# Optimization experiments

Measured on AMD Instinct MI355X. Metric: run time of the kernel, lower is better.

## Reference

```python
import jax, jax.numpy as jnp
import numpy as np

OC, IC, K, STRIDE, PAD, DIL, GROUPS = 256, 256, 3, 1, 1, 1, 1


def _conv_one(x, w):
    # x: [C, H, W], w: [OC, IC//groups, K, K]
    out = jax.lax.conv_general_dilated(
        x[None], w,
        window_strides=(STRIDE, STRIDE),
        padding=[(PAD, PAD), (PAD, PAD)],
        rhs_dilation=(DIL, DIL),
        dimension_numbers=("NCHW", "OIHW", "NCHW"),
        feature_group_count=GROUPS,
    )
    return out[0]  # [OC, H', W']


def setup_inputs() -> dict:
    key = jax.random.key(0)
    k1, k2, k3, k4 = jax.random.split(key, 4)
    B, num = 32, 64
    inputs = jax.random.normal(k1, (B, IC, 56, 56), dtype=jnp.float32)
    inputs_se = jax.random.normal(k2, (B, num), dtype=jnp.float32)
    fan = IC * K * K
    weight = jax.random.normal(k3, (OC * IC * K * K // GROUPS, num), dtype=jnp.float32) / np.sqrt(num * fan)
    bias = jax.random.normal(k4, (OC,), dtype=jnp.float32) * 0.01
    return {"inputs": inputs, "inputs_se": inputs_se, "weight": weight, "bias": bias}


def reference(inputs, inputs_se, weight, bias):
    B = inputs.shape[0]
    # per-sample weight synthesis: [B, OC*IC*K*K//groups]
    w = jnp.einsum("bn,on->bo", inputs_se, weight)
    w = w.reshape(B, OC, IC // GROUPS, K, K)
    out = jax.vmap(_conv_one)(inputs, w)  # [B, OC, H', W']
    return out + bias.reshape(1, -1, 1, 1)
```

## Files before the change

kernel.cpp:

```cpp
#include <hip/hip_runtime.h>

typedef __bf16 bf16x8 __attribute__((ext_vector_type(8)));
typedef float  f32x4  __attribute__((ext_vector_type(4)));

#define B_   32
#define OC   256
#define IC   256
#define HW   3136
#define HP   60
#define WP   58
#define KTOT 2304
#define XPAD_BYTES ((size_t)B_ * HP * WP * IC * 2)

#define SWZ(r) (((r) >> 1) & 3)

__device__ __forceinline__ void async16(const void* g, void* l) {
    __builtin_amdgcn_global_load_lds(
        (__attribute__((address_space(1))) void*)g,
        (__attribute__((address_space(3))) void*)l, 16, 0, 0);
}

__global__ __launch_bounds__(256) void zero_border(__bf16* __restrict__ Xpad) {
    int t   = blockIdx.x * 256 + threadIdx.x;
    int b   = t / 11008;
    int r2  = t - b * 11008;
    int pos = r2 >> 5, iq = r2 & 31;
    int r, c;
    if (pos < 232) { int rr = pos / 58; c = pos - rr * 58; r = (rr == 0) ? 0 : (56 + rr); }
    else           { int p2 = pos - 232; r = 1 + (p2 >> 1); c = (p2 & 1) * 57; }
    uint4 z = make_uint4(0u, 0u, 0u, 0u);
    *(uint4*)(Xpad + ((size_t)b * (HP * WP) + r * WP + c) * IC + iq * 8) = z;
}

__global__ __launch_bounds__(256) void transpose_pad(
    const float* __restrict__ X, __bf16* __restrict__ Xpad) {
    int sc = blockIdx.x, icc = blockIdx.y, b = blockIdx.z;
    __shared__ float lt[64][33];
    int tid = threadIdx.x;
    {
        int ci = tid >> 4, sq = tid & 15;
        const float* base = X + (size_t)(b * IC + icc * 32) * HW + sc * 64;
        float4 v0 = *(const float4*)(base + (size_t)ci * HW + sq * 4);
        float4 v1 = *(const float4*)(base + (size_t)(ci + 16) * HW + sq * 4);
        lt[sq * 4 + 0][ci] = v0.x; lt[sq * 4 + 1][ci] = v0.y;
        lt[sq * 4 + 2][ci] = v0.z; lt[sq * 4 + 3][ci] = v0.w;
        lt[sq * 4 + 0][ci + 16] = v1.x; lt[sq * 4 + 1][ci + 16] = v1.y;
        lt[sq * 4 + 2][ci + 16] = v1.z; lt[sq * 4 + 3][ci + 16] = v1.w;
    }
    __syncthreads();
    {
        int p = tid >> 2, iq = tid & 3;
        int s = sc * 64 + p;
        int h = s / 56, w = s - h * 56;
        __bf16* dst = Xpad + ((size_t)b * (HP * WP) + (h + 1) * WP + (w + 1)) * IC + icc * 32 + iq * 8;
        bf16x8 v;
        #pragma unroll
        for (int j = 0; j < 8; ++j) v[j] = (__bf16)lt[p][iq * 8 + j];
        *(bf16x8*)dst = v;
    }
}

__global__ __launch_bounds__(256) void synth(
    const float* __restrict__ se, const float* __restrict__ weight,
    __bf16* __restrict__ Asyn) {
    int oc = blockIdx.x / 9, tap = blockIdx.x - oc * 9;
    __shared__ float se_l[2048];
    int tid = threadIdx.x;
    #pragma unroll
    for (int i = 0; i < 2; ++i)
        ((float4*)se_l)[tid + i * 256] = ((const float4*)se)[tid + i * 256];
    __syncthreads();
    const float* wrow = weight + ((size_t)(oc * 256 + tid) * 9 + tap) * 64;
    float acc[32];
    #pragma unroll
    for (int b = 0; b < 32; ++b) acc[b] = 0.f;
    #pragma unroll
    for (int n4 = 0; n4 < 16; ++n4) {
        float4 w4 = *(const float4*)(wrow + n4 * 4);
        #pragma unroll
        for (int b = 0; b < 32; ++b) {
            float4 s4 = *(const float4*)(se_l + b * 64 + n4 * 4);
            acc[b] += w4.x * s4.x + w4.y * s4.y + w4.z * s4.z + w4.w * s4.w;
        }
    }
    size_t outb = (size_t)oc * KTOT + tap * 256 + tid;
    #pragma unroll
    for (int b = 0; b < 32; ++b)
        Asyn[(size_t)b * OC * KTOT + outb] = (__bf16)acc[b];
}

__global__ __launch_bounds__(256) void conv_mfma(
    const __bf16* __restrict__ Asyn, const __bf16* __restrict__ Xpad,
    const float* __restrict__ bias, float* __restrict__ Out) {
    const int ntile = blockIdx.x, mtile = blockIdx.y, b = blockIdx.z;
    __shared__ __bf16 Al[128 * 32];
    __shared__ __bf16 Bl[128 * 32];
    const int tid = threadIdx.x;
    const int wid = tid >> 6, lane = tid & 63;

    const int srow = lane >> 2, p = lane & 3;
    const int rl0 = wid * 32 + srow, rl1 = rl0 + 16;
    const int q0 = p ^ SWZ(rl0), q1 = p ^ SWZ(rl1);
    const __bf16* aptr0 = Asyn + (size_t)(b * OC + mtile * 128 + rl0) * KTOT + q0 * 8;
    const __bf16* aptr1 = Asyn + (size_t)(b * OC + mtile * 128 + rl1) * KTOT + q1 * 8;
    const int nn0 = ntile * 128 + rl0, nn1 = ntile * 128 + rl1;
    const int h0 = nn0 / 56, w0 = nn0 - h0 * 56;
    const int h1 = nn1 / 56, w1 = nn1 - h1 * 56;
    const __bf16* xb = Xpad + (size_t)b * (HP * WP) * IC;
    const __bf16* bptr0 = xb + ((h0 * WP) + w0) * IC + q0 * 8;
    const __bf16* bptr1 = xb + ((h1 * WP) + w1) * IC + q1 * 8;
    char* alds0 = (char*)Al + (wid * 32) * 64;
    char* alds1 = alds0 + 1024;
    char* blds0 = (char*)Bl + (wid * 32) * 64;
    char* blds1 = blds0 + 1024;

    const int wm = wid & 1, wn = wid >> 1;
    const int fr = lane & 15, fq = lane >> 4;
    int aoff[4], boff[4];
    #pragma unroll
    for (int i = 0; i < 4; ++i) {
        int ra = wm * 64 + i * 16 + fr;
        aoff[i] = ra * 32 + (fq ^ SWZ(ra)) * 8;
        int rb = wn * 64 + i * 16 + fr;
        boff[i] = rb * 32 + (fq ^ SWZ(rb)) * 8;
    }
    f32x4 acc[4][4] = {};

    for (int tap = 0; tap < 9; ++tap) {
        const int kh = tap / 3, kw = tap - kh * 3;
        const int bo = (kh * WP + kw) * IC;
        const int ko = tap * 256;
        for (int icc = 0; icc < 8; ++icc) {
            const int kk = ko + icc * 32;
            async16(aptr0 + kk, alds0);
            async16(aptr1 + kk, alds1);
            async16(bptr0 + bo + icc * 32, blds0);
            async16(bptr1 + bo + icc * 32, blds1);
            __syncthreads();
            bf16x8 af[4], bv[4];
            #pragma unroll
            for (int i = 0; i < 4; ++i) {
                af[i] = *(const bf16x8*)(Al + aoff[i]);
                bv[i] = *(const bf16x8*)(Bl + boff[i]);
            }
            #pragma unroll
            for (int mi = 0; mi < 4; ++mi)
                #pragma unroll
                for (int ni = 0; ni < 4; ++ni)
                    acc[mi][ni] = __builtin_amdgcn_mfma_f32_16x16x32_bf16(
                        af[mi], bv[ni], acc[mi][ni], 0, 0, 0);
            __syncthreads();
        }
    }

    #pragma unroll
    for (int mi = 0; mi < 4; ++mi) {
        #pragma unroll
        for (int r = 0; r < 4; ++r) {
            const int row = mtile * 128 + wm * 64 + mi * 16 + fq * 4 + r;
            const float bvv = bias[row];
            float* orow = Out + (size_t)(b * OC + row) * HW;
            #pragma unroll
            for (int ni = 0; ni < 4; ++ni) {
                const int col = ntile * 128 + wn * 64 + ni * 16 + fr;
                if (col < HW) orow[col] = acc[mi][ni][r] + bvv;
            }
        }
    }
}

extern "C" void kernel_launch(void* const* d_in, const int* in_sizes, int n_in,
                              void* d_out, int out_size, void* d_ws, size_t ws_size,
                              hipStream_t stream) {
    const float* X    = (const float*)d_in[0];
    const float* se   = (const float*)d_in[1];
    const float* Wt   = (const float*)d_in[2];
    const float* bias = (const float*)d_in[3];
    __bf16* Xpad = (__bf16*)d_ws;
    __bf16* Asyn = (__bf16*)((char*)d_ws + XPAD_BYTES);
    float*  Out  = (float*)d_out;

    zero_border<<<1376, 256, 0, stream>>>(Xpad);
    transpose_pad<<<dim3(49, 8, 32), 256, 0, stream>>>(X, Xpad);
    synth<<<2304, 256, 0, stream>>>(se, Wt, Asyn);
    conv_mfma<<<dim3(25, 2, 32), 256, 0, stream>>>(Asyn, Xpad, bias, Out);
}
```

Measured before the change: 563.0 us.

## Remap conv blocks per XCD, widen transpose tiles, register-cache synth weights

The conv grid is flattened to 1600 blocks, and block indices are remapped so that all tiles of a given batch sample land on the same XCD, which should improve L2 reuse of that sample's Xpad and Asyn data. The transpose kernel now handles 64 channels per block, using four float4 loads per thread and 16-element stores. The synth kernel keeps each weight row in registers and reads se directly from global memory instead of staging it in LDS. These changes add register pressure in synth and move the transpose's strided access onto LDS reads.

```diff
diff --git a/kernel.cpp b/kernel.cpp
--- a/kernel.cpp
+++ b/kernel.cpp
@@ -35,28 +35,32 @@
 __global__ __launch_bounds__(256) void transpose_pad(
     const float* __restrict__ X, __bf16* __restrict__ Xpad) {
     int sc = blockIdx.x, icc = blockIdx.y, b = blockIdx.z;
-    __shared__ float lt[64][33];
+    __shared__ float lt[64][65];
     int tid = threadIdx.x;
     {
-        int ci = tid >> 4, sq = tid & 15;
-        const float* base = X + (size_t)(b * IC + icc * 32) * HW + sc * 64;
-        float4 v0 = *(const float4*)(base + (size_t)ci * HW + sq * 4);
-        float4 v1 = *(const float4*)(base + (size_t)(ci + 16) * HW + sq * 4);
-        lt[sq * 4 + 0][ci] = v0.x; lt[sq * 4 + 1][ci] = v0.y;
-        lt[sq * 4 + 2][ci] = v0.z; lt[sq * 4 + 3][ci] = v0.w;
-        lt[sq * 4 + 0][ci + 16] = v1.x; lt[sq * 4 + 1][ci + 16] = v1.y;
-        lt[sq * 4 + 2][ci + 16] = v1.z; lt[sq * 4 + 3][ci + 16] = v1.w;
+        int ci = tid >> 2, sq = tid & 3;
+        const float* src = X + (size_t)(b * IC + icc * 64 + ci) * HW + sc * 64 + sq * 16;
+        float4 v0 = ((const float4*)src)[0];
+        float4 v1 = ((const float4*)src)[1];
+        float4 v2 = ((const float4*)src)[2];
+        float4 v3 = ((const float4*)src)[3];
+        float* dst = &lt[ci][sq * 16];
+        ((float4*)dst)[0] = v0; ((float4*)dst)[1] = v1;
+        ((float4*)dst)[2] = v2; ((float4*)dst)[3] = v3;
     }
     __syncthreads();
     {
         int p = tid >> 2, iq = tid & 3;
         int s = sc * 64 + p;
         int h = s / 56, w = s - h * 56;
-        __bf16* dst = Xpad + ((size_t)b * (HP * WP) + (h + 1) * WP + (w + 1)) * IC + icc * 32 + iq * 8;
-        bf16x8 v;
+        __bf16* dst = Xpad + ((size_t)b * (HP * WP) + (h + 1) * WP + (w + 1)) * IC + icc * 64 + iq * 16;
+        bf16x8 v0, v1;
         #pragma unroll
-        for (int j = 0; j < 8; ++j) v[j] = (__bf16)lt[p][iq * 8 + j];
-        *(bf16x8*)dst = v;
+        for (int j = 0; j < 8; ++j) v0[j] = (__bf16)lt[iq * 16 + j][p];
+        #pragma unroll
+        for (int j = 0; j < 8; ++j) v1[j] = (__bf16)lt[iq * 16 + 8 + j][p];
+        *(bf16x8*)dst = v0;
+        *(bf16x8*)(dst + 8) = v1;
     }
 }
 
@@ -64,35 +68,34 @@
     const float* __restrict__ se, const float* __restrict__ weight,
     __bf16* __restrict__ Asyn) {
     int oc = blockIdx.x / 9, tap = blockIdx.x - oc * 9;
-    __shared__ float se_l[2048];
     int tid = threadIdx.x;
+    const float* wrow = weight + ((size_t)(oc * 256 + tid) * 9 + tap) * 64;
+    float4 w[16];
     #pragma unroll
-    for (int i = 0; i < 2; ++i)
-        ((float4*)se_l)[tid + i * 256] = ((const float4*)se)[tid + i * 256];
-    __syncthreads();
-    const float* wrow = weight + ((size_t)(oc * 256 + tid) * 9 + tap) * 64;
-    float acc[32];
-    #pragma unroll
-    for (int b = 0; b < 32; ++b) acc[b] = 0.f;
-    #pragma unroll
-    for (int n4 = 0; n4 < 16; ++n4) {
-        float4 w4 = *(const float4*)(wrow + n4 * 4);
-        #pragma unroll
-        for (int b = 0; b < 32; ++b) {
-            float4 s4 = *(const float4*)(se_l + b * 64 + n4 * 4);
-            acc[b] += w4.x * s4.x + w4.y * s4.y + w4.z * s4.z + w4.w * s4.w;
-        }
-    }
+    for (int i = 0; i < 16; ++i) w[i] = ((const float4*)wrow)[i];
     size_t outb = (size_t)oc * KTOT + tap * 256 + tid;
     #pragma unroll
-    for (int b = 0; b < 32; ++b)
-        Asyn[(size_t)b * OC * KTOT + outb] = (__bf16)acc[b];
+    for (int b = 0; b < 32; ++b) {
+        const float4* sb = (const float4*)(se + b * 64);
+        float acc = 0.f;
+        #pragma unroll
+        for (int i = 0; i < 16; ++i) {
+            float4 s4 = sb[i];
+            acc += w[i].x * s4.x + w[i].y * s4.y + w[i].z * s4.z + w[i].w * s4.w;
+        }
+        Asyn[(size_t)b * OC * KTOT + outb] = (__bf16)acc;
+    }
 }
 
 __global__ __launch_bounds__(256) void conv_mfma(
     const __bf16* __restrict__ Asyn, const __bf16* __restrict__ Xpad,
     const float* __restrict__ bias, float* __restrict__ Out) {
-    const int ntile = blockIdx.x, mtile = blockIdx.y, b = blockIdx.z;
+    const int i = blockIdx.x;
+    const int xcd = i & 7, slot = i >> 3;
+    const int bg = slot / 50, r2 = slot - bg * 50;
+    const int b = xcd + 8 * bg;
+    const int mtile = r2 & 1, ntile = r2 >> 1;
+
     __shared__ __bf16 Al[128 * 32];
     __shared__ __bf16 Bl[128 * 32];
     const int tid = threadIdx.x;
@@ -118,11 +121,11 @@
     const int fr = lane & 15, fq = lane >> 4;
     int aoff[4], boff[4];
     #pragma unroll
-    for (int i = 0; i < 4; ++i) {
-        int ra = wm * 64 + i * 16 + fr;
-        aoff[i] = ra * 32 + (fq ^ SWZ(ra)) * 8;
-        int rb = wn * 64 + i * 16 + fr;
-        boff[i] = rb * 32 + (fq ^ SWZ(rb)) * 8;
+    for (int i2 = 0; i2 < 4; ++i2) {
+        int ra = wm * 64 + i2 * 16 + fr;
+        aoff[i2] = ra * 32 + (fq ^ SWZ(ra)) * 8;
+        int rb = wn * 64 + i2 * 16 + fr;
+        boff[i2] = rb * 32 + (fq ^ SWZ(rb)) * 8;
     }
     f32x4 acc[4][4] = {};
 
@@ -139,9 +142,9 @@
             __syncthreads();
             bf16x8 af[4], bv[4];
             #pragma unroll
-            for (int i = 0; i < 4; ++i) {
-                af[i] = *(const bf16x8*)(Al + aoff[i]);
-                bv[i] = *(const bf16x8*)(Bl + boff[i]);
+            for (int i2 = 0; i2 < 4; ++i2) {
+                af[i2] = *(const bf16x8*)(Al + aoff[i2]);
+                bv[i2] = *(const bf16x8*)(Bl + boff[i2]);
             }
             #pragma unroll
             for (int mi = 0; mi < 4; ++mi)
@@ -181,7 +184,7 @@
     float*  Out  = (float*)d_out;
 
     zero_border<<<1376, 256, 0, stream>>>(Xpad);
-    transpose_pad<<<dim3(49, 8, 32), 256, 0, stream>>>(X, Xpad);
+    transpose_pad<<<dim3(49, 4, 32), 256, 0, stream>>>(X, Xpad);
     synth<<<2304, 256, 0, stream>>>(se, Wt, Asyn);
-    conv_mfma<<<dim3(25, 2, 32), 256, 0, stream>>>(Asyn, Xpad, bias, Out);
+    conv_mfma<<<1600, 256, 0, stream>>>(Asyn, Xpad, bias, Out);
 }
```

After: 523.9 us. 7.0% less time.
